# Optimization experiments

Hardware: AMD Instinct MI355X
Metric: run time of the kernel (lower is better)

## Reference

```python
import jax, jax.numpy as jnp
import numpy as np

H = 2048   # hidden_dim
E = 8      # num_experts
K = 2      # top_k
N = 4096   # tokens


def setup_inputs() -> dict:
    key = jax.random.key(0)
    ks = jax.random.split(key, 8)
    scale = 0.02
    return {
        "x": jax.random.normal(ks[0], (N, H), dtype=jnp.float32),
        # gate: torch Linear(H, E) -> weight [E, H], bias [E]
        "gate_W": jax.random.normal(ks[1], (E, H), dtype=jnp.float32) * scale,
        "gate_b": jnp.zeros((E,), dtype=jnp.float32),
        # per-expert 2-layer MLP; stored as [E, in, out] for direct einsum
        "W1": jax.random.normal(ks[2], (E, H, H), dtype=jnp.float32) * scale,
        "b1": jnp.zeros((E, H), dtype=jnp.float32),
        "W2": jax.random.normal(ks[3], (E, H, H), dtype=jnp.float32) * scale,
        "b2": jnp.zeros((E, H), dtype=jnp.float32),
    }


def reference(x, gate_W, gate_b, W1, b1, W2, b2):
    # gate softmax over experts: [N, E]
    gate_scores = jax.nn.softmax(x @ gate_W.T + gate_b, axis=-1)
    topk_scores, topk_idx = jax.lax.top_k(gate_scores, K)  # [N, K]
    n = x.shape[0]
    # combine weights: score at selected experts, 0 elsewhere -> [N, E]
    combine = jnp.zeros_like(gate_scores).at[
        jnp.arange(n)[:, None], topk_idx
    ].set(topk_scores)
    # dense per-expert MLP: h [N, E, H]
    h = jax.nn.relu(jnp.einsum('nh,ehf->nef', x, W1) + b1)
    out_e = jnp.einsum('nef,efg->neg', h, W2) + b2  # [N, E, H]
    aggregated = jnp.einsum('ne,neh->nh', combine, out_e)  # [N, H]
    return aggregated, gate_scores
```

## Files before the change

### kernel.cpp

```cpp
#include <hip/hip_runtime.h>
#include <hip/hip_bf16.h>

#define N_TOK 4096
#define HD    2048
#define NE    8

#define BM 128
#define BN 256
#define BK 32
#define NKS (HD/BK)
#define MAXROWS (N_TOK*2 + NE*BM)
#define TMAX (MAXROWS/BM)
#define NNT  (HD/BN)
#define NWG  (TMAX*NNT)
#define TSZ  ((BM+BN)*BK*2)

#define NCOPY 64
#define NCVT  4096

typedef __attribute__((ext_vector_type(4))) float f32x4;
typedef __attribute__((ext_vector_type(8))) short short8;
typedef __attribute__((ext_vector_type(8))) unsigned short ushort8;

typedef unsigned short u16;
typedef unsigned int   u32;


__device__ __forceinline__ float bf2f(u16 u) {
  union { u32 i; float f; } c; c.i = ((u32)u) << 16; return c.f;
}
__device__ __forceinline__ u16 f2bf(float f) {
  u32 x = __float_as_uint(f);
  u32 r = (x + 0x7fffu + ((x >> 16) & 1u)) >> 16;
  return (u16)r;
}

__device__ __forceinline__ void gload_lds16(const void* gsrc, void* ldst) {
  __builtin_amdgcn_global_load_lds(
      (const __attribute__((address_space(1))) u32*)gsrc,
      (__attribute__((address_space(3))) u32*)ldst, 16, 0, 0);
}

__global__ __launch_bounds__(256) void convert_gate_kernel(
    const float* __restrict__ W1, const float* __restrict__ W2,
    u16* __restrict__ W1T, u16* __restrict__ W2T,
    const float* __restrict__ x, const float* __restrict__ gW,
    const float* __restrict__ gb, float* __restrict__ gate_out,
    int* __restrict__ cnt, int* __restrict__ picks, float* __restrict__ wts) {
  __shared__ float smem[NE*HD];
  int b = blockIdx.x;
  int t = threadIdx.x;

  if (b < NCVT) {
    f32x4* tile4 = reinterpret_cast<f32x4*>(smem);
    int bx = b & 7, by = (b >> 3) & 31, z = b >> 8;
    const float* W = (z < NE) ? W1 : W2;
    u16* WT = (z < NE) ? W1T : W2T;
    int e = z & 7;
    size_t ebase = (size_t)e * HD * HD;
    int n0 = bx * 256;
    int k0 = by * 64;
    int l = t & 63, w = t >> 6;
    #pragma unroll
    for (int i = 0; i < 16; ++i) {
      int r = i*4 + w;
      f32x4 v = *reinterpret_cast<const f32x4*>(W + ebase + (size_t)(k0 + r) * HD + n0 + l*4);
      tile4[r*64 + (l ^ (r & 7))] = v;
    }
    __syncthreads();
    #pragma unroll
    for (int i = 0; i < 8; ++i) {
      int np = i*32 + (t >> 3);
      int kc = (t & 7) * 8;
      int c4 = np >> 2, inner = np & 3;
      ushort8 v;
      #pragma unroll
      for (int j = 0; j < 8; ++j) {
        int k = kc + j;
        v[j] = f2bf(smem[(k*64 + (c4 ^ (k & 7)))*4 + inner]);
      }
      *reinterpret_cast<ushort8*>(WT + ebase + (size_t)(n0 + np) * HD + k0 + kc) = v;
    }
  } else {
    float* gwl = smem;
    int gbk = b - NCVT;
    {
      const f32x4* g4 = reinterpret_cast<const f32x4*>(gW);
      f32x4* l4 = reinterpret_cast<f32x4*>(gwl);
      #pragma unroll
      for (int i = 0; i < 16; ++i) l4[i*256 + t] = g4[i*256 + t];
    }
    __syncthreads();
    int wid = (gbk << 2) + (t >> 6);
    int lane = t & 63;
    int copy = gbk & (NCOPY-1);
    const float* xr = x + (size_t)wid * HD;
    float s[NE] = {};
    for (int k = 0; k < HD; k += 256) {
      f32x4 xv = *reinterpret_cast<const f32x4*>(xr + k + lane*4);
      #pragma unroll
      for (int e = 0; e < NE; ++e) {
        f32x4 wv = *reinterpret_cast<const f32x4*>(&gwl[e*HD + k + lane*4]);
        s[e] += xv[0]*wv[0] + xv[1]*wv[1] + xv[2]*wv[2] + xv[3]*wv[3];
      }
    }
    #pragma unroll
    for (int e = 0; e < NE; ++e) {
      float v = s[e];
      #pragma unroll
      for (int off = 32; off > 0; off >>= 1) v += __shfl_xor(v, off);
      s[e] = v + gb[e];
    }
    float mx = s[0];
    #pragma unroll
    for (int e = 1; e < NE; ++e) mx = fmaxf(mx, s[e]);
    float sum = 0.f;
    #pragma unroll
    for (int e = 0; e < NE; ++e) { s[e] = expf(s[e] - mx); sum += s[e]; }
    float inv = 1.f / sum;
    #pragma unroll
    for (int e = 0; e < NE; ++e) s[e] *= inv;
    int e0 = 0; float v0 = s[0];
    #pragma unroll
    for (int e = 1; e < NE; ++e) if (s[e] > v0) { v0 = s[e]; e0 = e; }
    int e1 = -1; float v1 = -1.f;
    #pragma unroll
    for (int e = 0; e < NE; ++e) if (e != e0 && s[e] > v1) { v1 = s[e]; e1 = e; }
    if (lane == 0) {
      #pragma unroll
      for (int e = 0; e < NE; ++e) gate_out[(size_t)wid*NE + e] = s[e];
      int p0 = atomicAdd(&cnt[copy*8 + e0], 1);
      int p1 = atomicAdd(&cnt[copy*8 + e1], 1);
      picks[wid*2]   = (p0 << 9) | (copy << 3) | e0;
      picks[wid*2+1] = (p1 << 9) | (copy << 3) | e1;
      wts[wid*2]   = v0;
      wts[wid*2+1] = v1;
    }
  }
}

__global__ void scan_kernel(int* meta) {
  int e = threadIdx.x;
  if (e < NE) {
    int run = 0;
    for (int c = 0; c < NCOPY; ++c) {
      meta[512 + c*8 + e] = run;
      run += meta[c*8 + e];
    }
    meta[1024 + e] = run;
  }
}

__global__ void fill_kernel(const int* __restrict__ picks, const int* __restrict__ meta,
                            int* __restrict__ slot, int* __restrict__ rowTok) {
  int i = blockIdx.x * 256 + threadIdx.x;
  if (i >= N_TOK*2) return;
  int p = picks[i];
  int e = p & 7, c = (p >> 3) & (NCOPY-1), pos = p >> 9;
  int base = 0;
  #pragma unroll
  for (int ee = 0; ee < NE; ++ee)
    if (ee < e) base += ((meta[1024+ee] + BM - 1) >> 7) << 7;
  int row = base + meta[512 + c*8 + e] + pos;
  slot[i] = row;
  rowTok[row] = i >> 1;
}

__global__ __launch_bounds__(256) void gather_kernel(
    const float* __restrict__ x, const int* __restrict__ rowTok,
    u16* __restrict__ Xg) {
  int row = blockIdx.x;
  int tok = rowTok[row];
  int c = threadIdx.x * 8;
  ushort8 v;
  if (tok >= 0) {
    const f32x4* src = reinterpret_cast<const f32x4*>(x + (size_t)tok * HD + c);
    f32x4 a = src[0], b = src[1];
    #pragma unroll
    for (int j = 0; j < 4; ++j) { v[j] = f2bf(a[j]); v[4+j] = f2bf(b[j]); }
  } else {
    #pragma unroll
    for (int j = 0; j < 8; ++j) v[j] = 0;
  }
  *reinterpret_cast<ushort8*>(Xg + (size_t)row * HD + c) = v;
}

__device__ __forceinline__ void stage_tile(char* ldsbuf, const u16* Ak, const u16* Bk, int tid) {
  {
    int r = tid >> 2;
    int c = (tid & 3) ^ ((r >> 1) & 3);
    gload_lds16(Ak + (size_t)r*HD + c*8, ldsbuf + tid*16);
  }
  #pragma unroll
  for (int i = 0; i < 2; ++i) {
    int L = i*512 + tid;
    int r = L >> 2;
    int c = (L & 3) ^ ((r >> 1) & 3);
    gload_lds16(Bk + (size_t)r*HD + c*8, ldsbuf + BM*BK*2 + L*16);
  }
}

__device__ __forceinline__ void compute_ktile(
    const char* ldsA, const char* ldsB, f32x4 (&acc)[4][4],
    int wr, int wc, int l15, int lhi) {
  short8 af[4], bfr[4];
  #pragma unroll
  for (int m = 0; m < 4; ++m) {
    int r = wr*64 + m*16 + l15;
    int c = lhi ^ ((r >> 1) & 3);
    af[m] = *reinterpret_cast<const short8*>(ldsA + r*64 + c*16);
  }
  #pragma unroll
  for (int n = 0; n < 4; ++n) {
    int r = wc*64 + n*16 + l15;
    int c = lhi ^ ((r >> 1) & 3);
    bfr[n] = *reinterpret_cast<const short8*>(ldsB + r*64 + c*16);
  }
  #pragma unroll
  for (int m = 0; m < 4; ++m)
    #pragma unroll
    for (int n = 0; n < 4; ++n)
      acc[m][n] = __builtin_amdgcn_mfma_f32_16x16x32_bf16(af[m], bfr[n], acc[m][n], 0, 0, 0);
}

template<bool RELU>
__global__ __launch_bounds__(512, 4) void moe_gemm_kernel(
    const u16* __restrict__ A,
    const u16* __restrict__ WT,
    const float* __restrict__ bias,
    u16* __restrict__ Out,
    const int* __restrict__ tot) {
  int bid = blockIdx.x;
  int wg = (bid & 7) * (NWG/8) + (bid >> 3);
  int t  = wg >> 3;
  int nt = wg & 7;
  int tiles = 0, rows = 0, e = 0, tstart = 0, rbase = 0;
  #pragma unroll
  for (int i = 0; i < NE; ++i) {
    int tl = (tot[i] + BM - 1) >> 7;
    if (t >= tiles && t < tiles + tl) { e = i; tstart = tiles; rbase = rows; }
    tiles += tl; rows += tl << 7;
  }
  if (t >= tiles) return;
  int rowBase = rbase + (t - tstart) * BM;

  const u16* Ap = A + (size_t)rowBase * HD;
  const u16* Bp = WT + ((size_t)e * HD + (size_t)nt * BN) * HD;

  __shared__ char lds[3*TSZ];

  int tid = threadIdx.x;
  int lane = tid & 63;
  int wv = tid >> 6;
  int wr = wv >> 2, wc = wv & 3;
  int l15 = lane & 15, lhi = lane >> 4;

  f32x4 acc[4][4] = {};

  stage_tile(lds,       Ap,      Bp,      tid);
  stage_tile(lds + TSZ, Ap + BK, Bp + BK, tid);

  int rd = 0;
  for (int ks = 0; ks < NKS - 2; ++ks) {
    asm volatile("s_waitcnt vmcnt(3)" ::: "memory");
    __builtin_amdgcn_s_barrier();
    int wi = rd + 2; if (wi >= 3) wi -= 3;
    stage_tile(lds + wi*TSZ, Ap + (ks+2)*BK, Bp + (ks+2)*BK, tid);
    __builtin_amdgcn_sched_barrier(0);
    compute_ktile(lds + rd*TSZ, lds + rd*TSZ + BM*BK*2, acc, wr, wc, l15, lhi);
    if (++rd == 3) rd = 0;
  }
  asm volatile("s_waitcnt vmcnt(3)" ::: "memory");
  __builtin_amdgcn_s_barrier();
  compute_ktile(lds + rd*TSZ, lds + rd*TSZ + BM*BK*2, acc, wr, wc, l15, lhi);
  if (++rd == 3) rd = 0;
  asm volatile("s_waitcnt vmcnt(0)" ::: "memory");
  __builtin_amdgcn_s_barrier();
  compute_ktile(lds + rd*TSZ, lds + rd*TSZ + BM*BK*2, acc, wr, wc, l15, lhi);

  int orow = rowBase + wr*64;
  int ocol = nt*BN + wc*64;
  const float* bp = bias + (size_t)e * HD + ocol;
  #pragma unroll
  for (int n = 0; n < 4; ++n) {
    float bv = bp[n*16 + l15];
    #pragma unroll
    for (int m = 0; m < 4; ++m) {
      #pragma unroll
      for (int j = 0; j < 4; ++j) {
        float v = acc[m][n][j] + bv;
        if (RELU) v = fmaxf(v, 0.f);
        Out[(size_t)(orow + m*16 + lhi*4 + j) * HD + (ocol + n*16 + l15)] = f2bf(v);
      }
    }
  }
}

__global__ __launch_bounds__(256) void combine_kernel(
    const u16* __restrict__ Y, const int* __restrict__ slot,
    const float* __restrict__ wts, float* __restrict__ out) {
  int n = blockIdx.x;
  int r0 = slot[n*2], r1 = slot[n*2+1];
  float w0 = wts[n*2], w1 = wts[n*2+1];
  int c = threadIdx.x * 8;
  ushort8 y0 = *reinterpret_cast<const ushort8*>(Y + (size_t)r0*HD + c);
  ushort8 y1 = *reinterpret_cast<const ushort8*>(Y + (size_t)r1*HD + c);
  f32x4 o0, o1;
  #pragma unroll
  for (int j = 0; j < 4; ++j) {
    o0[j] = w0*bf2f(y0[j])   + w1*bf2f(y1[j]);
    o1[j] = w0*bf2f(y0[4+j]) + w1*bf2f(y1[4+j]);
  }
  f32x4* dst = reinterpret_cast<f32x4*>(out + (size_t)n*HD + c);
  dst[0] = o0; dst[1] = o1;
}

extern "C" void kernel_launch(void* const* d_in, const int* in_sizes, int n_in,
                              void* d_out, int out_size, void* d_ws, size_t ws_size,
                              hipStream_t stream) {
  const float* x     = (const float*)d_in[0];
  const float* gateW = (const float*)d_in[1];
  const float* gateb = (const float*)d_in[2];
  const float* W1    = (const float*)d_in[3];
  const float* b1    = (const float*)d_in[4];
  const float* W2    = (const float*)d_in[5];
  const float* b2    = (const float*)d_in[6];
  float* out      = (float*)d_out;
  float* gate_out = out + (size_t)N_TOK * HD;

  char* ws = (char*)d_ws;
  size_t o = 0;
  u16* W1T = (u16*)(ws + o); o += (size_t)NE*HD*HD*2;
  u16* W2T = (u16*)(ws + o); o += (size_t)NE*HD*HD*2;
  u16* Xg  = (u16*)(ws + o);
  u16* Y   = Xg;
  o += (size_t)MAXROWS*HD*2;
  u16* Hbuf = (u16*)(ws + o); o += (size_t)MAXROWS*HD*2;
  int*   meta   = (int*)(ws + o);   o += 8192;
  int*   picks  = (int*)(ws + o);   o += (size_t)N_TOK*2*4;
  float* wts    = (float*)(ws + o); o += (size_t)N_TOK*2*4;
  int*   slot   = (int*)(ws + o);   o += (size_t)N_TOK*2*4;
  int*   rowTok = (int*)(ws + o);   o += (size_t)MAXROWS*4;

  hipMemsetAsync(meta, 0, NCOPY*8*4, stream);
  hipMemsetAsync(rowTok, 0xFF, (size_t)MAXROWS*4, stream);

  convert_gate_kernel<<<dim3(NCVT + N_TOK/4), 256, 0, stream>>>(
      W1, W2, W1T, W2T, x, gateW, gateb, gate_out, meta, picks, wts);
  scan_kernel<<<1, 64, 0, stream>>>(meta);
  fill_kernel<<<(N_TOK*2)/256, 256, 0, stream>>>(picks, meta, slot, rowTok);
  gather_kernel<<<MAXROWS, 256, 0, stream>>>(x, rowTok, Xg);
  moe_gemm_kernel<true ><<<dim3(NWG), 512, 0, stream>>>(Xg,   W1T, b1, Hbuf, meta + 1024);
  moe_gemm_kernel<false><<<dim3(NWG), 512, 0, stream>>>(Hbuf, W2T, b2, Y,    meta + 1024);
  combine_kernel<<<N_TOK, 256, 0, stream>>>(Y, slot, wts, out);
}
```

Measured before the change: 313.5 us.

## Fuse token gather into first expert GEMM via indirect row loads

Removes the separate gather kernel. x is now converted to bf16 densely inside the convert/gate kernel, and the first GEMM reads A rows indirectly through rowTok. Padding rows are clamped to token 0, and their outputs are discarded. The LDS swizzle in the weight transpose also changes from row&7 to (row>>3)&7, which changes the bank-conflict pattern. This saves one launch and the gathered copy, but the A-tile loads become scattered rows.

```diff
diff --git a/kernel.cpp b/kernel.cpp
--- a/kernel.cpp
+++ b/kernel.cpp
@@ -17,6 +17,8 @@
 
 #define NCOPY 64
 #define NCVT  4096
+#define NGATE (N_TOK/4)
+#define NXCV  (N_TOK*HD/2048)
 
 typedef __attribute__((ext_vector_type(4))) float f32x4;
 typedef __attribute__((ext_vector_type(8))) short short8;
@@ -46,12 +48,21 @@
     u16* __restrict__ W1T, u16* __restrict__ W2T,
     const float* __restrict__ x, const float* __restrict__ gW,
     const float* __restrict__ gb, float* __restrict__ gate_out,
-    int* __restrict__ cnt, int* __restrict__ picks, float* __restrict__ wts) {
+    int* __restrict__ cnt, int* __restrict__ picks, float* __restrict__ wts,
+    u16* __restrict__ Xbf) {
   __shared__ float smem[NE*HD];
   int b = blockIdx.x;
   int t = threadIdx.x;
 
-  if (b < NCVT) {
+  if (b >= NCVT + NGATE) {
+    size_t base = (size_t)(b - NCVT - NGATE) * 2048 + (size_t)t * 8;
+    f32x4 a = *reinterpret_cast<const f32x4*>(x + base);
+    f32x4 c = *reinterpret_cast<const f32x4*>(x + base + 4);
+    ushort8 v;
+    #pragma unroll
+    for (int j = 0; j < 4; ++j) { v[j] = f2bf(a[j]); v[4+j] = f2bf(c[j]); }
+    *reinterpret_cast<ushort8*>(Xbf + base) = v;
+  } else if (b < NCVT) {
     f32x4* tile4 = reinterpret_cast<f32x4*>(smem);
     int bx = b & 7, by = (b >> 3) & 31, z = b >> 8;
     const float* W = (z < NE) ? W1 : W2;
@@ -65,7 +76,7 @@
     for (int i = 0; i < 16; ++i) {
       int r = i*4 + w;
       f32x4 v = *reinterpret_cast<const f32x4*>(W + ebase + (size_t)(k0 + r) * HD + n0 + l*4);
-      tile4[r*64 + (l ^ (r & 7))] = v;
+      tile4[r*64 + (l ^ ((r >> 3) & 7))] = v;
     }
     __syncthreads();
     #pragma unroll
@@ -77,7 +88,7 @@
       #pragma unroll
       for (int j = 0; j < 8; ++j) {
         int k = kc + j;
-        v[j] = f2bf(smem[(k*64 + (c4 ^ (k & 7)))*4 + inner]);
+        v[j] = f2bf(smem[(k*64 + (c4 ^ ((k >> 3) & 7)))*4 + inner]);
       }
       *reinterpret_cast<ushort8*>(WT + ebase + (size_t)(n0 + np) * HD + k0 + kc) = v;
     }
@@ -166,40 +177,6 @@
   rowTok[row] = i >> 1;
 }
 
-__global__ __launch_bounds__(256) void gather_kernel(
-    const float* __restrict__ x, const int* __restrict__ rowTok,
-    u16* __restrict__ Xg) {
-  int row = blockIdx.x;
-  int tok = rowTok[row];
-  int c = threadIdx.x * 8;
-  ushort8 v;
-  if (tok >= 0) {
-    const f32x4* src = reinterpret_cast<const f32x4*>(x + (size_t)tok * HD + c);
-    f32x4 a = src[0], b = src[1];
-    #pragma unroll
-    for (int j = 0; j < 4; ++j) { v[j] = f2bf(a[j]); v[4+j] = f2bf(b[j]); }
-  } else {
-    #pragma unroll
-    for (int j = 0; j < 8; ++j) v[j] = 0;
-  }
-  *reinterpret_cast<ushort8*>(Xg + (size_t)row * HD + c) = v;
-}
-
-__device__ __forceinline__ void stage_tile(char* ldsbuf, const u16* Ak, const u16* Bk, int tid) {
-  {
-    int r = tid >> 2;
-    int c = (tid & 3) ^ ((r >> 1) & 3);
-    gload_lds16(Ak + (size_t)r*HD + c*8, ldsbuf + tid*16);
-  }
-  #pragma unroll
-  for (int i = 0; i < 2; ++i) {
-    int L = i*512 + tid;
-    int r = L >> 2;
-    int c = (L & 3) ^ ((r >> 1) & 3);
-    gload_lds16(Bk + (size_t)r*HD + c*8, ldsbuf + BM*BK*2 + L*16);
-  }
-}
-
 __device__ __forceinline__ void compute_ktile(
     const char* ldsA, const char* ldsB, f32x4 (&acc)[4][4],
     int wr, int wc, int l15, int lhi) {
@@ -223,13 +200,14 @@
       acc[m][n] = __builtin_amdgcn_mfma_f32_16x16x32_bf16(af[m], bfr[n], acc[m][n], 0, 0, 0);
 }
 
-template<bool RELU>
+template<bool RELU, bool IND>
 __global__ __launch_bounds__(512, 4) void moe_gemm_kernel(
     const u16* __restrict__ A,
     const u16* __restrict__ WT,
     const float* __restrict__ bias,
     u16* __restrict__ Out,
-    const int* __restrict__ tot) {
+    const int* __restrict__ tot,
+    const int* __restrict__ rowTok) {
   int bid = blockIdx.x;
   int wg = (bid & 7) * (NWG/8) + (bid >> 3);
   int t  = wg >> 3;
@@ -244,7 +222,6 @@
   if (t >= tiles) return;
   int rowBase = rbase + (t - tstart) * BM;
 
-  const u16* Ap = A + (size_t)rowBase * HD;
   const u16* Bp = WT + ((size_t)e * HD + (size_t)nt * BN) * HD;
 
   __shared__ char lds[3*TSZ];
@@ -255,17 +232,42 @@
   int wr = wv >> 2, wc = wv & 3;
   int l15 = lane & 15, lhi = lane >> 4;
 
+  int aR = tid >> 2;
+  int aC = (tid & 3) ^ ((aR >> 1) & 3);
+  const u16* Asrc;
+  if (IND) {
+    int tk = rowTok[rowBase + aR];
+    if (tk < 0) tk = 0;
+    Asrc = A + (size_t)tk * HD + aC*8;
+  } else {
+    Asrc = A + (size_t)(rowBase + aR) * HD + aC*8;
+  }
+  int b1R = 128 + aR;
+  int b1C = (tid & 3) ^ ((b1R >> 1) & 3);
+  const u16* Bsrc0 = Bp + (size_t)aR * HD + aC*8;
+  const u16* Bsrc1 = Bp + (size_t)b1R * HD + b1C*8;
+  int ldsAoff = tid*16;
+  int ldsB0off = BM*BK*2 + tid*16;
+  int ldsB1off = BM*BK*2 + (512 + tid)*16;
+
   f32x4 acc[4][4] = {};
 
-  stage_tile(lds,       Ap,      Bp,      tid);
-  stage_tile(lds + TSZ, Ap + BK, Bp + BK, tid);
+  gload_lds16(Asrc,       lds + ldsAoff);
+  gload_lds16(Bsrc0,      lds + ldsB0off);
+  gload_lds16(Bsrc1,      lds + ldsB1off);
+  gload_lds16(Asrc  + BK, lds + TSZ + ldsAoff);
+  gload_lds16(Bsrc0 + BK, lds + TSZ + ldsB0off);
+  gload_lds16(Bsrc1 + BK, lds + TSZ + ldsB1off);
 
   int rd = 0;
   for (int ks = 0; ks < NKS - 2; ++ks) {
     asm volatile("s_waitcnt vmcnt(3)" ::: "memory");
     __builtin_amdgcn_s_barrier();
     int wi = rd + 2; if (wi >= 3) wi -= 3;
-    stage_tile(lds + wi*TSZ, Ap + (ks+2)*BK, Bp + (ks+2)*BK, tid);
+    int koff = (ks+2)*BK;
+    gload_lds16(Asrc  + koff, lds + wi*TSZ + ldsAoff);
+    gload_lds16(Bsrc0 + koff, lds + wi*TSZ + ldsB0off);
+    gload_lds16(Bsrc1 + koff, lds + wi*TSZ + ldsB1off);
     __builtin_amdgcn_sched_barrier(0);
     compute_ktile(lds + rd*TSZ, lds + rd*TSZ + BM*BK*2, acc, wr, wc, l15, lhi);
     if (++rd == 3) rd = 0;
@@ -332,8 +334,8 @@
   size_t o = 0;
   u16* W1T = (u16*)(ws + o); o += (size_t)NE*HD*HD*2;
   u16* W2T = (u16*)(ws + o); o += (size_t)NE*HD*HD*2;
-  u16* Xg  = (u16*)(ws + o);
-  u16* Y   = Xg;
+  u16* Xbf = (u16*)(ws + o);
+  u16* Y   = Xbf;
   o += (size_t)MAXROWS*HD*2;
   u16* Hbuf = (u16*)(ws + o); o += (size_t)MAXROWS*HD*2;
   int*   meta   = (int*)(ws + o);   o += 8192;
@@ -345,12 +347,13 @@
   hipMemsetAsync(meta, 0, NCOPY*8*4, stream);
   hipMemsetAsync(rowTok, 0xFF, (size_t)MAXROWS*4, stream);
 
-  convert_gate_kernel<<<dim3(NCVT + N_TOK/4), 256, 0, stream>>>(
-      W1, W2, W1T, W2T, x, gateW, gateb, gate_out, meta, picks, wts);
+  convert_gate_kernel<<<dim3(NCVT + NGATE + NXCV), 256, 0, stream>>>(
+      W1, W2, W1T, W2T, x, gateW, gateb, gate_out, meta, picks, wts, Xbf);
   scan_kernel<<<1, 64, 0, stream>>>(meta);
   fill_kernel<<<(N_TOK*2)/256, 256, 0, stream>>>(picks, meta, slot, rowTok);
-  gather_kernel<<<MAXROWS, 256, 0, stream>>>(x, rowTok, Xg);
-  moe_gemm_kernel<true ><<<dim3(NWG), 512, 0, stream>>>(Xg,   W1T, b1, Hbuf, meta + 1024);
-  moe_gemm_kernel<false><<<dim3(NWG), 512, 0, stream>>>(Hbuf, W2T, b2, Y,    meta + 1024);
+  moe_gemm_kernel<true,  true ><<<dim3(NWG), 512, 0, stream>>>(Xbf,  W1T, b1, Hbuf,
+                                                               meta + 1024, rowTok);
+  moe_gemm_kernel<false, false><<<dim3(NWG), 512, 0, stream>>>(Hbuf, W2T, b2, Y,
+                                                               meta + 1024, rowTok);
   combine_kernel<<<N_TOK, 256, 0, stream>>>(Y, slot, wts, out);
 }
```

Measured after the change: 304.4 us. -2.9%, faster.
